# Kernel optimization log

Measured on AMD Instinct MI355X. Metric: run time of the kernel, lower is better.

Reference implementation:

```python
import jax, jax.numpy as jnp
import numpy as np

ALPHA = 0.5
BETA = 0.25
D_AGG = 0.5          # delta_aggregation
D_DIS = 3.0          # delta_discrimination
OHEM_RATIO = 3.0
MAX_INST = 8         # max instance label (labels in 1..MAX_INST, 0 = background)
SMOOTH = 1e-3


def _aggr_discr(text, kernel, embed):
    # text, kernel: [HW] int32 instance labels; embed: [4, HW] float
    inst = jnp.arange(1, MAX_INST + 1)                              # [I]
    kmask = (kernel[None, :] == inst[:, None]).astype(embed.dtype)  # [I, HW]
    tmask = (text[None, :] == inst[:, None]).astype(embed.dtype)   # [I, HW]
    kcnt = kmask.sum(1)                                             # [I]
    tcnt = tmask.sum(1)
    valid = ((kcnt > 0) & (tcnt > 0)).astype(embed.dtype)           # [I]
    # per-instance kernel-mean embedding (segment mean)
    avgs = (kmask @ embed.T) / jnp.maximum(kcnt, 1.0)[:, None]      # [I, 4]
    # aggregation: per-pixel distance to the mean of its text instance
    avgs_full = jnp.concatenate([jnp.zeros((1, 4), embed.dtype), avgs], 0)  # row 0 = bg
    pix_avg = avgs_full[text]                                       # [HW, 4]
    sq = jnp.sum((embed.T - pix_avg) ** 2, axis=1)
    dist = jnp.sqrt(sq + 1e-12) - D_AGG
    lg = jnp.log1p(jnp.maximum(dist, 0.0) ** 2)                     # [HW]
    aggr_i = (tmask @ lg) / jnp.maximum(tcnt, 1.0)                  # [I]
    n = valid.sum()
    loss_aggr = jnp.where(n > 0, (aggr_i * valid).sum() / jnp.maximum(n, 1.0), 0.0)
    # discrimination: pairwise hinge between valid kernel means
    pairv = jnp.triu(valid[:, None] * valid[None, :], k=1)          # [I, I]
    sq_ij = jnp.sum((avgs[:, None, :] - avgs[None, :, :]) ** 2, axis=-1)
    d_ij = jnp.sqrt(jnp.where(pairv > 0, sq_ij, 1.0))               # safe sqrt
    L = jnp.log1p(jnp.maximum(D_DIS - d_ij, 0.0) ** 2)
    denom = n * (n - 1)
    loss_discr = jnp.where(n > 1, (L * pairv).sum() / jnp.maximum(denom, 1.0), 0.0)
    return loss_aggr, loss_discr


def _ohem(score, gt_text, gt_mask):
    # score, gt_text, gt_mask: [HW] float
    pos = gt_text > 0.5
    maskpos = gt_mask > 0.5
    pos_num = (pos & maskpos).sum()
    neg = ~pos
    neg_num = jnp.minimum((pos_num * OHEM_RATIO).astype(jnp.int32), neg.sum())
    neg_sc = jnp.where(neg, score, -jnp.inf)
    srt = -jnp.sort(-neg_sc)                                        # descending
    thr = srt[jnp.clip(neg_num - 1, 0, score.shape[0] - 1)]
    samp = ((score >= thr) | pos) & maskpos
    fallback = (pos_num == 0) | (neg_num == 0)
    return jnp.where(fallback, maskpos, samp).astype(score.dtype)


def _dice(pred_logits, target, mask):
    # all [N, HW]
    p = jax.nn.sigmoid(pred_logits) * mask
    t = (target > 0.5).astype(p.dtype) * mask
    a = jnp.sum(p * t, 1) + SMOOTH
    b = jnp.sum(p * p, 1) + SMOOTH
    c = jnp.sum(t * t, 1) + SMOOTH
    return 1.0 - 2.0 * a / (b + c)


def reference(preds, gt_texts, gt_kernels, gt_mask):
    N, C, H, W = preds.shape
    HW = H * W
    pred_text = preds[:, 0].reshape(N, HW)
    pred_kernel = preds[:, 1].reshape(N, HW)
    embed = preds[:, 2:].reshape(N, 4, HW)
    t = gt_texts.reshape(N, HW)
    k = gt_kernels.reshape(N, HW)
    m = gt_mask.reshape(N, HW).astype(preds.dtype)
    tf = t.astype(preds.dtype)
    kf = k.astype(preds.dtype)
    loss_aggr, loss_discr = jax.vmap(_aggr_discr)(t, k, embed)
    samp = jax.vmap(_ohem)(jax.lax.stop_gradient(pred_text), tf, m)
    loss_text = _dice(pred_text, tf, samp)
    samp_k = (tf > 0.5).astype(preds.dtype) * m
    loss_kernel = _dice(pred_kernel, kf, samp_k)
    # reduction='mean' then coefs [1, alpha, beta, beta]
    return jnp.stack([
        loss_text.mean(),
        ALPHA * loss_kernel.mean(),
        BETA * loss_aggr.mean(),
        BETA * loss_discr.mean(),
    ])


def setup_inputs() -> dict:
    key = jax.random.key(0)
    k1, k2, k3, k4 = jax.random.split(key, 4)
    N, H, W = 16, 512, 512
    preds = jax.random.normal(k1, (N, 6, H, W), dtype=jnp.float32)
    gt_texts = jax.random.randint(k2, (N, H, W), 0, 9, dtype=jnp.int32)
    gt_kernels = jax.random.randint(k3, (N, H, W), 0, 9, dtype=jnp.int32)
    gt_mask = jax.random.randint(k4, (N, H, W), 0, 2, dtype=jnp.int32)
    return {"preds": preds, "gt_texts": gt_texts, "gt_kernels": gt_kernels, "gt_mask": gt_mask}
```

## Files before the change

kernel.cpp:

```cpp
#include <hip/hip_runtime.h>
#include <math.h>

#define HW (512 * 512)
#define NB 16
#define NTHR 256
#define GXS_S 128
#define CH_S 2
#define GXS_P 64
#define CH_P 4
#define ACCW 56

#define OFF_ACC    0
#define OFF_PPART  (OFF_ACC + NB * GXS_S * ACCW)
#define OFF_KDICE  (OFF_PPART + NB * GXS_P * 4)
#define OFF_NVAL   (OFF_KDICE + NB * 3)
#define OFF_DISCR  (OFF_NVAL + NB)


__device__ __forceinline__ unsigned fmap(float f) {
    unsigned u = __float_as_uint(f);
    return (u & 0x80000000u) ? ~u : (u | 0x80000000u);
}
__device__ __forceinline__ float funmap(unsigned u) {
    return (u & 0x80000000u) ? __uint_as_float(u & 0x7FFFFFFFu)
                             : __uint_as_float(~u);
}
__device__ __forceinline__ float wred(float x) {
#pragma unroll
    for (int o = 32; o; o >>= 1) x += __shfl_xor(x, o);
    return x;
}
__device__ __forceinline__ unsigned long long wredull(unsigned long long x) {
#pragma unroll
    for (int o = 32; o; o >>= 1)
        x += (unsigned long long)__shfl_xor((unsigned long long)x, o);
    return x;
}

__global__ __launch_bounds__(NTHR, 2) void k_stats(const float* __restrict__ preds,
                        const int* __restrict__ text,
                        const int* __restrict__ kern,
                        const int* __restrict__ mask,
                        unsigned* __restrict__ wsu) {
    float* wsf = (float*)wsu;
    const int b = blockIdx.y;
    const int tid = threadIdx.x;
    const int lane = tid & 63;
    __shared__ float sacc[53];
    if (tid < 53) sacc[tid] = 0.f;
    __syncthreads();

    const int* tb = text + b * HW;
    const int* kb = kern + b * HW;
    const int* mb = mask + b * HW;
    const float* p1 = preds + (size_t)(b * 6 + 1) * HW;
    const float* e0 = preds + (size_t)(b * 6 + 2) * HW;
    const float* e1 = e0 + HW;
    const float* e2 = e0 + 2 * HW;
    const float* e3 = e0 + 3 * HW;

    unsigned negc = 0u;

    float ks[32];
#pragma unroll
    for (int i = 0; i < 32; i++) ks[i] = 0.f;
    float r_ak = 0.f, r_bk = 0.f, r_ck = 0.f, r_pos = 0.f;
    unsigned kcW[8] = {0, 0, 0, 0, 0, 0, 0, 0};
    unsigned long long tpack = 0ull;

#pragma unroll 1
    for (int c = 0; c < CH_S; c++) {
        const int base = blockIdx.x * (NTHR * 4 * CH_S) + c * (NTHR * 4) + tid * 4;
        const int4 t4 = *(const int4*)(tb + base);
        const int4 k4 = *(const int4*)(kb + base);
        const int4 m4 = *(const int4*)(mb + base);
        const float4 q4 = *(const float4*)(p1 + base);
        const float4 a4 = *(const float4*)(e0 + base);
        const float4 b4 = *(const float4*)(e1 + base);
        const float4 c4 = *(const float4*)(e2 + base);
        const float4 d4 = *(const float4*)(e3 + base);

#define PIX(T, K, M, Q, A, B, C, D) do {                                     \
        bool pos_ = (T) > 0, mp_ = (M) > 0;                                  \
        float sm_ = (pos_ && mp_) ? 1.f : 0.f;                               \
        float sg_ = 1.f / (1.f + expf(-(Q)));                                \
        float ik_ = ((K) > 0) ? 1.f : 0.f;                                   \
        r_ak += sm_ * sg_ * ik_;                                             \
        r_bk += sm_ * sg_ * sg_;                                             \
        r_ck += sm_ * ik_;                                                   \
        r_pos += sm_;                                                        \
        tpack += pos_ ? (1ull << ((((unsigned)(T) - 1u) & 7u) * 8u)) : 0ull; \
        _Pragma("unroll")                                                    \
        for (int i_ = 0; i_ < 8; i_++) {                                     \
            bool hit_ = ((K) == i_ + 1);                                     \
            kcW[i_] += (unsigned)__popcll(__ballot(hit_));                   \
            float h_ = hit_ ? 1.f : 0.f;                                     \
            ks[i_ * 4 + 0] += h_ * (A);                                      \
            ks[i_ * 4 + 1] += h_ * (B);                                      \
            ks[i_ * 4 + 2] += h_ * (C);                                      \
            ks[i_ * 4 + 3] += h_ * (D);                                      \
        }                                                                    \
    } while (0)

        PIX(t4.x, k4.x, m4.x, q4.x, a4.x, b4.x, c4.x, d4.x);
        PIX(t4.y, k4.y, m4.y, q4.y, a4.y, b4.y, c4.y, d4.y);
        PIX(t4.z, k4.z, m4.z, q4.z, a4.z, b4.z, c4.z, d4.z);
        PIX(t4.w, k4.w, m4.w, q4.w, a4.w, b4.w, c4.w, d4.w);
#undef PIX

        negc += (unsigned)(t4.x == 0) + (unsigned)(t4.y == 0)
              + (unsigned)(t4.z == 0) + (unsigned)(t4.w == 0);
    }

#pragma unroll
    for (int i = 0; i < 32; i++) {
        float v = wred(ks[i]);
        if (lane == 0) atomicAdd(&sacc[16 + i], v);
    }
    {
        float v = wred(r_ak); if (lane == 0) atomicAdd(&sacc[49], v);
        v = wred(r_bk); if (lane == 0) atomicAdd(&sacc[50], v);
        v = wred(r_ck); if (lane == 0) atomicAdd(&sacc[51], v);
        v = wred(r_pos); if (lane == 0) atomicAdd(&sacc[48], v);
        unsigned nv = negc;
#pragma unroll
        for (int o = 32; o; o >>= 1) nv += (unsigned)__shfl_xor((int)nv, o);
        if (lane == 0) atomicAdd(&sacc[52], (float)nv);
    }
    {
        unsigned long long lo = tpack & 0x00FF00FF00FF00FFull;
        unsigned long long hi = (tpack >> 8) & 0x00FF00FF00FF00FFull;
        lo = wredull(lo);
        hi = wredull(hi);
        if (lane == 0) {
            atomicAdd(&sacc[8 + 0], (float)(unsigned)( lo        & 0xFFFFull));
            atomicAdd(&sacc[8 + 2], (float)(unsigned)((lo >> 16) & 0xFFFFull));
            atomicAdd(&sacc[8 + 4], (float)(unsigned)((lo >> 32) & 0xFFFFull));
            atomicAdd(&sacc[8 + 6], (float)(unsigned)((lo >> 48) & 0xFFFFull));
            atomicAdd(&sacc[8 + 1], (float)(unsigned)( hi        & 0xFFFFull));
            atomicAdd(&sacc[8 + 3], (float)(unsigned)((hi >> 16) & 0xFFFFull));
            atomicAdd(&sacc[8 + 5], (float)(unsigned)((hi >> 32) & 0xFFFFull));
            atomicAdd(&sacc[8 + 7], (float)(unsigned)((hi >> 48) & 0xFFFFull));
        }
    }
    if (lane == 0) {
#pragma unroll
        for (int i = 0; i < 8; i++) atomicAdd(&sacc[i], (float)kcW[i]);
    }
    __syncthreads();
    if (tid < 53)
        wsf[OFF_ACC + (b * GXS_S + blockIdx.x) * ACCW + tid] = sacc[tid];
}

__global__ __launch_bounds__(NTHR, 2) void k_pix(const float* __restrict__ preds,
                      const int* __restrict__ text,
                      const int* __restrict__ mask,
                      unsigned* __restrict__ wsu) {
    float* wsf = (float*)wsu;
    const int b = blockIdx.y;
    const int tid = threadIdx.x;
    const int lane = tid & 63;
    __shared__ float s_sum[53];
    __shared__ float stbl[45];
    __shared__ int s_valid[8];
    __shared__ float s_thr;
    __shared__ int s_uni;
    __shared__ unsigned s_kk, s_prefix;
    __shared__ unsigned s_hist[256];
    __shared__ float sred[4];

    const int* tb = text + b * HW;
    const int* mb = mask + b * HW;
    const float* p0 = preds + (size_t)(b * 6) * HW;
    const float* e0 = preds + (size_t)(b * 6 + 2) * HW;
    const float* e1 = e0 + HW;
    const float* e2 = e0 + 2 * HW;
    const float* e3 = e0 + 3 * HW;

    if (tid < 53) {
        float v = 0.f;
        const float* p = wsf + OFF_ACC + (size_t)b * GXS_S * ACCW + tid;
        for (int r = 0; r < GXS_S; r++) v += p[r * ACCW];
        s_sum[tid] = v;
    }
    if (tid < 4) sred[tid] = 0.f;
    __syncthreads();
    if (tid < 8) {
        float kcf = s_sum[tid];
        float tcf = s_sum[8 + tid];
        int valid = (kcf > 0.f && tcf > 0.f) ? 1 : 0;
        s_valid[tid] = valid;
        float inv = 1.f / fmaxf(kcf, 1.f);
        float w = valid ? 1.f / fmaxf(tcf, 1.f) : 0.f;
#pragma unroll
        for (int c = 0; c < 4; c++)
            stbl[(tid + 1) * 5 + c] = s_sum[16 + tid * 4 + c] * inv;
        stbl[(tid + 1) * 5 + 4] = w;
    }
    if (tid >= 8 && tid < 13) stbl[tid - 8] = 0.f;
    __syncthreads();
    if (tid == 0) {
        unsigned pos = (unsigned)s_sum[48];
        unsigned neg = (unsigned)s_sum[52];
        unsigned nn = min(pos * 3u, neg);
        int uni = (pos == 0u || nn == 0u || nn == neg) ? 1 : 0;
        s_uni = uni;
        s_kk = uni ? 0u : nn;
        s_thr = 0.f;
        s_prefix = 0u;
    }
    if (blockIdx.x == 0) {
        if (tid >= 16 && tid < 19)
            wsf[OFF_KDICE + b * 3 + (tid - 16)] = s_sum[49 + (tid - 16)];
        if (tid == 32) {
            int nval = 0;
            for (int i = 0; i < 8; i++) nval += s_valid[i];
            wsu[OFF_NVAL + b] = (unsigned)nval;
            float L = 0.f;
            for (int i = 0; i < 8; i++)
                for (int j = i + 1; j < 8; j++)
                    if (s_valid[i] && s_valid[j]) {
                        float sq = 0.f;
                        for (int c = 0; c < 4; c++) {
                            float d = stbl[(i + 1) * 5 + c] - stbl[(j + 1) * 5 + c];
                            sq += d * d;
                        }
                        float h = fmaxf(3.0f - sqrtf(sq), 0.f);
                        L += log1pf(h * h);
                    }
            wsf[OFF_DISCR + b] = (nval > 1) ? L / fmaxf((float)(nval * (nval - 1)), 1.f) : 0.f;
        }
    }
    __syncthreads();
    if (s_kk != 0u) {
        unsigned prefix = 0u;
        for (int pass = 0; pass < 4; pass++) {
            const int shift = 24 - 8 * pass;
            const unsigned fmask = (pass == 0) ? 0u : (0xFFFFFFFFu << (shift + 8));
            s_hist[tid] = 0u;
            __syncthreads();
            for (int p = tid; p < HW; p += NTHR) {
                if (tb[p] == 0) {
                    unsigned key = fmap(p0[p]);
                    if ((key & fmask) == prefix) atomicAdd(&s_hist[(key >> shift) & 255u], 1u);
                }
            }
            __syncthreads();
            if (tid == 0) {
                unsigned k2 = s_kk;
                for (int bin = 255; bin >= 0; --bin) {
                    unsigned c = s_hist[bin];
                    if (k2 <= c) { s_prefix = prefix | (((unsigned)bin) << shift); s_kk = k2; break; }
                    k2 -= c;
                }
            }
            __syncthreads();
            prefix = s_prefix;
        }
        if (tid == 0) s_thr = funmap(prefix);
        __syncthreads();
    }
    const float thr = s_thr;
    const bool uni = s_uni != 0;

    float r_at = 0.f, r_bt = 0.f, r_ct = 0.f, r_ag = 0.f;
#pragma unroll 1
    for (int c = 0; c < CH_P; c++) {
        const int base = blockIdx.x * (NTHR * 4 * CH_P) + c * (NTHR * 4) + tid * 4;
        const int4 t4 = *(const int4*)(tb + base);
        const int4 m4 = *(const int4*)(mb + base);
        const float4 s4 = *(const float4*)(p0 + base);
        const float4 a4 = *(const float4*)(e0 + base);
        const float4 b4 = *(const float4*)(e1 + base);
        const float4 c4 = *(const float4*)(e2 + base);
        const float4 d4 = *(const float4*)(e3 + base);

#define PPIX(T, M, S, A, B, C, D) do {                                       \
        bool pos_ = (T) > 0;                                                 \
        bool samp_ = uni ? ((M) > 0) : ((((S) >= thr) || pos_) && ((M) > 0)); \
        float sg_ = 1.f / (1.f + expf(-(S)));                                \
        float smf_ = samp_ ? 1.f : 0.f;                                      \
        float it_ = pos_ ? 1.f : 0.f;                                        \
        r_at += smf_ * sg_ * it_;                                            \
        r_bt += smf_ * sg_ * sg_;                                            \
        r_ct += smf_ * it_;                                                  \
        int t5_ = min((T), 8) * 5;                                           \
        float d0_ = (A) - stbl[t5_ + 0];                                     \
        float d1_ = (B) - stbl[t5_ + 1];                                     \
        float d2_ = (C) - stbl[t5_ + 2];                                     \
        float d3_ = (D) - stbl[t5_ + 3];                                     \
        float w_ = stbl[t5_ + 4];                                            \
        float sq_ = d0_ * d0_ + d1_ * d1_ + d2_ * d2_ + d3_ * d3_;           \
        float dist_ = sqrtf(sq_ + 1e-12f) - 0.5f;                            \
        float hp_ = fmaxf(dist_, 0.f);                                       \
        r_ag += w_ * log1pf(hp_ * hp_);                                      \
    } while (0)

        PPIX(t4.x, m4.x, s4.x, a4.x, b4.x, c4.x, d4.x);
        PPIX(t4.y, m4.y, s4.y, a4.y, b4.y, c4.y, d4.y);
        PPIX(t4.z, m4.z, s4.z, a4.z, b4.z, c4.z, d4.z);
        PPIX(t4.w, m4.w, s4.w, a4.w, b4.w, c4.w, d4.w);
#undef PPIX
    }

    {
        float v = wred(r_at); if (lane == 0) atomicAdd(&sred[0], v);
        v = wred(r_bt); if (lane == 0) atomicAdd(&sred[1], v);
        v = wred(r_ct); if (lane == 0) atomicAdd(&sred[2], v);
        v = wred(r_ag); if (lane == 0) atomicAdd(&sred[3], v);
    }
    __syncthreads();
    if (tid < 4)
        wsf[OFF_PPART + (b * GXS_P + blockIdx.x) * 4 + tid] = sred[tid];
}

__global__ void k_final(unsigned* __restrict__ wsu, float* __restrict__ out) {
    float* wsf = (float*)wsu;
    __shared__ float sfin[64];
    __shared__ float lt[NB], lk[NB], la[NB], ld[NB];
    const int tid = threadIdx.x;
    {
        const int bb = tid >> 2, v = tid & 3;
        float s = 0.f;
        const float* p = wsf + OFF_PPART + (size_t)bb * GXS_P * 4 + v;
        for (int r = 0; r < GXS_P; r++) s += p[r * 4];
        sfin[tid] = s;
    }
    __syncthreads();
    if (tid < NB) {
        const float S = 1e-3f;
        float at = sfin[tid * 4 + 0], bt = sfin[tid * 4 + 1];
        float ct = sfin[tid * 4 + 2], ag = sfin[tid * 4 + 3];
        float ak = wsf[OFF_KDICE + tid * 3 + 0];
        float bk = wsf[OFF_KDICE + tid * 3 + 1];
        float ck = wsf[OFF_KDICE + tid * 3 + 2];
        lt[tid] = 1.f - 2.f * (at + S) / ((bt + S) + (ct + S));
        lk[tid] = 1.f - 2.f * (ak + S) / ((bk + S) + (ck + S));
        int nval = (int)wsu[OFF_NVAL + tid];
        la[tid] = (nval > 0) ? ag / fmaxf((float)nval, 1.f) : 0.f;
        ld[tid] = wsf[OFF_DISCR + tid];
    }
    __syncthreads();
    if (tid == 0) {
        float st = 0, sk = 0, sa = 0, sd = 0;
        for (int i = 0; i < NB; i++) { st += lt[i]; sk += lk[i]; sa += la[i]; sd += ld[i]; }
        out[0] = st / NB;
        out[1] = 0.5f * sk / NB;
        out[2] = 0.25f * sa / NB;
        out[3] = 0.25f * sd / NB;
    }
}

extern "C" void kernel_launch(void* const* d_in, const int* in_sizes, int n_in,
                              void* d_out, int out_size, void* d_ws, size_t ws_size,
                              hipStream_t stream) {
    const float* preds = (const float*)d_in[0];
    const int* text = (const int*)d_in[1];
    const int* kern = (const int*)d_in[2];
    const int* mask = (const int*)d_in[3];
    unsigned* wsu = (unsigned*)d_ws;
    float* out = (float*)d_out;

    dim3 grid_s(GXS_S, NB);
    dim3 grid_p(GXS_P, NB);
    k_stats<<<grid_s, NTHR, 0, stream>>>(preds, text, kern, mask, wsu);
    k_pix<<<grid_p, NTHR, 0, stream>>>(preds, text, mask, wsu);
    k_final<<<1, 64, 0, stream>>>(wsu, out);
}
```

Before: 228.3 us.

## Move text dice sums into stats pass when OHEM selects all negatives

The text-dice partial sums for the case where OHEM keeps every masked pixel are now computed in the first stats kernel, which reads the text score channel in addition to its other inputs. The second pixel kernel gets a branch for that case that only loads text labels and embeddings for the aggregation term, skipping the mask and score loads and the sigmoid. The final kernel adds the precomputed text-dice sums from a new workspace slot. In exchange, the stats kernel does an extra channel load and a second sigmoid per pixel on every input, including inputs that take the non-uniform path.

Measured after the change: 233.1 us. 2.1% more time.

```diff
diff --git a/kernel.cpp b/kernel.cpp
--- a/kernel.cpp
+++ b/kernel.cpp
@@ -13,7 +13,8 @@
 #define OFF_ACC    0
 #define OFF_PPART  (OFF_ACC + NB * GXS_S * ACCW)
 #define OFF_KDICE  (OFF_PPART + NB * GXS_P * 4)
-#define OFF_NVAL   (OFF_KDICE + NB * 3)
+#define OFF_TDICE  (OFF_KDICE + NB * 3)
+#define OFF_NVAL   (OFF_TDICE + NB * 3)
 #define OFF_DISCR  (OFF_NVAL + NB)
 
 
@@ -46,13 +47,14 @@
     const int b = blockIdx.y;
     const int tid = threadIdx.x;
     const int lane = tid & 63;
-    __shared__ float sacc[53];
-    if (tid < 53) sacc[tid] = 0.f;
+    __shared__ float sacc[55];
+    if (tid < 55) sacc[tid] = 0.f;
     __syncthreads();
 
     const int* tb = text + b * HW;
     const int* kb = kern + b * HW;
     const int* mb = mask + b * HW;
+    const float* p0 = preds + (size_t)(b * 6 + 0) * HW;
     const float* p1 = preds + (size_t)(b * 6 + 1) * HW;
     const float* e0 = preds + (size_t)(b * 6 + 2) * HW;
     const float* e1 = e0 + HW;
@@ -65,6 +67,7 @@
 #pragma unroll
     for (int i = 0; i < 32; i++) ks[i] = 0.f;
     float r_ak = 0.f, r_bk = 0.f, r_ck = 0.f, r_pos = 0.f;
+    float r_at = 0.f, r_bt = 0.f;
     unsigned kcW[8] = {0, 0, 0, 0, 0, 0, 0, 0};
     unsigned long long tpack = 0ull;
 
@@ -74,21 +77,26 @@
         const int4 t4 = *(const int4*)(tb + base);
         const int4 k4 = *(const int4*)(kb + base);
         const int4 m4 = *(const int4*)(mb + base);
+        const float4 s4 = *(const float4*)(p0 + base);
         const float4 q4 = *(const float4*)(p1 + base);
         const float4 a4 = *(const float4*)(e0 + base);
         const float4 b4 = *(const float4*)(e1 + base);
         const float4 c4 = *(const float4*)(e2 + base);
         const float4 d4 = *(const float4*)(e3 + base);
 
-#define PIX(T, K, M, Q, A, B, C, D) do {                                     \
+#define PIX(T, K, M, Q, S, A, B, C, D) do {                                  \
         bool pos_ = (T) > 0, mp_ = (M) > 0;                                  \
         float sm_ = (pos_ && mp_) ? 1.f : 0.f;                               \
+        float mpf_ = mp_ ? 1.f : 0.f;                                        \
         float sg_ = 1.f / (1.f + expf(-(Q)));                                \
+        float sg0_ = 1.f / (1.f + expf(-(S)));                               \
         float ik_ = ((K) > 0) ? 1.f : 0.f;                                   \
         r_ak += sm_ * sg_ * ik_;                                             \
         r_bk += sm_ * sg_ * sg_;                                             \
         r_ck += sm_ * ik_;                                                   \
         r_pos += sm_;                                                        \
+        r_at += sm_ * sg0_;                                                  \
+        r_bt += mpf_ * sg0_ * sg0_;                                          \
         tpack += pos_ ? (1ull << ((((unsigned)(T) - 1u) & 7u) * 8u)) : 0ull; \
         _Pragma("unroll")                                                    \
         for (int i_ = 0; i_ < 8; i_++) {                                     \
@@ -102,10 +110,10 @@
         }                                                                    \
     } while (0)
 
-        PIX(t4.x, k4.x, m4.x, q4.x, a4.x, b4.x, c4.x, d4.x);
-        PIX(t4.y, k4.y, m4.y, q4.y, a4.y, b4.y, c4.y, d4.y);
-        PIX(t4.z, k4.z, m4.z, q4.z, a4.z, b4.z, c4.z, d4.z);
-        PIX(t4.w, k4.w, m4.w, q4.w, a4.w, b4.w, c4.w, d4.w);
+        PIX(t4.x, k4.x, m4.x, q4.x, s4.x, a4.x, b4.x, c4.x, d4.x);
+        PIX(t4.y, k4.y, m4.y, q4.y, s4.y, a4.y, b4.y, c4.y, d4.y);
+        PIX(t4.z, k4.z, m4.z, q4.z, s4.z, a4.z, b4.z, c4.z, d4.z);
+        PIX(t4.w, k4.w, m4.w, q4.w, s4.w, a4.w, b4.w, c4.w, d4.w);
 #undef PIX
 
         negc += (unsigned)(t4.x == 0) + (unsigned)(t4.y == 0)
@@ -122,6 +130,8 @@
         v = wred(r_bk); if (lane == 0) atomicAdd(&sacc[50], v);
         v = wred(r_ck); if (lane == 0) atomicAdd(&sacc[51], v);
         v = wred(r_pos); if (lane == 0) atomicAdd(&sacc[48], v);
+        v = wred(r_at); if (lane == 0) atomicAdd(&sacc[53], v);
+        v = wred(r_bt); if (lane == 0) atomicAdd(&sacc[54], v);
         unsigned nv = negc;
 #pragma unroll
         for (int o = 32; o; o >>= 1) nv += (unsigned)__shfl_xor((int)nv, o);
@@ -148,7 +158,7 @@
         for (int i = 0; i < 8; i++) atomicAdd(&sacc[i], (float)kcW[i]);
     }
     __syncthreads();
-    if (tid < 53)
+    if (tid < 55)
         wsf[OFF_ACC + (b * GXS_S + blockIdx.x) * ACCW + tid] = sacc[tid];
 }
 
@@ -160,7 +170,7 @@
     const int b = blockIdx.y;
     const int tid = threadIdx.x;
     const int lane = tid & 63;
-    __shared__ float s_sum[53];
+    __shared__ float s_sum[55];
     __shared__ float stbl[45];
     __shared__ int s_valid[8];
     __shared__ float s_thr;
@@ -177,7 +187,7 @@
     const float* e2 = e0 + 2 * HW;
     const float* e3 = e0 + 3 * HW;
 
-    if (tid < 53) {
+    if (tid < 55) {
         float v = 0.f;
         const float* p = wsf + OFF_ACC + (size_t)b * GXS_S * ACCW + tid;
         for (int r = 0; r < GXS_S; r++) v += p[r * ACCW];
@@ -209,9 +219,15 @@
         s_thr = 0.f;
         s_prefix = 0u;
     }
+    __syncthreads();
     if (blockIdx.x == 0) {
         if (tid >= 16 && tid < 19)
             wsf[OFF_KDICE + b * 3 + (tid - 16)] = s_sum[49 + (tid - 16)];
+        if (tid >= 20 && tid < 23) {
+            const int idx[3] = {53, 54, 48};
+            wsf[OFF_TDICE + b * 3 + (tid - 20)] =
+                s_uni ? s_sum[idx[tid - 20]] : 0.f;
+        }
         if (tid == 32) {
             int nval = 0;
             for (int i = 0; i < 8; i++) nval += s_valid[i];
@@ -264,20 +280,50 @@
     const bool uni = s_uni != 0;
 
     float r_at = 0.f, r_bt = 0.f, r_ct = 0.f, r_ag = 0.f;
+    if (uni) {
 #pragma unroll 1
-    for (int c = 0; c < CH_P; c++) {
-        const int base = blockIdx.x * (NTHR * 4 * CH_P) + c * (NTHR * 4) + tid * 4;
-        const int4 t4 = *(const int4*)(tb + base);
-        const int4 m4 = *(const int4*)(mb + base);
-        const float4 s4 = *(const float4*)(p0 + base);
-        const float4 a4 = *(const float4*)(e0 + base);
-        const float4 b4 = *(const float4*)(e1 + base);
-        const float4 c4 = *(const float4*)(e2 + base);
-        const float4 d4 = *(const float4*)(e3 + base);
+        for (int c = 0; c < CH_P; c++) {
+            const int base = blockIdx.x * (NTHR * 4 * CH_P) + c * (NTHR * 4) + tid * 4;
+            const int4 t4 = *(const int4*)(tb + base);
+            const float4 a4 = *(const float4*)(e0 + base);
+            const float4 b4 = *(const float4*)(e1 + base);
+            const float4 c4 = *(const float4*)(e2 + base);
+            const float4 d4 = *(const float4*)(e3 + base);
+
+#define AGPIX(T, A, B, C, D) do {                                            \
+        int t5_ = min((T), 8) * 5;                                           \
+        float d0_ = (A) - stbl[t5_ + 0];                                     \
+        float d1_ = (B) - stbl[t5_ + 1];                                     \
+        float d2_ = (C) - stbl[t5_ + 2];                                     \
+        float d3_ = (D) - stbl[t5_ + 3];                                     \
+        float w_ = stbl[t5_ + 4];                                            \
+        float sq_ = d0_ * d0_ + d1_ * d1_ + d2_ * d2_ + d3_ * d3_;           \
+        float dist_ = sqrtf(sq_ + 1e-12f) - 0.5f;                            \
+        float hp_ = fmaxf(dist_, 0.f);                                       \
+        r_ag += w_ * log1pf(hp_ * hp_);                                      \
+    } while (0)
+
+            AGPIX(t4.x, a4.x, b4.x, c4.x, d4.x);
+            AGPIX(t4.y, a4.y, b4.y, c4.y, d4.y);
+            AGPIX(t4.z, a4.z, b4.z, c4.z, d4.z);
+            AGPIX(t4.w, a4.w, b4.w, c4.w, d4.w);
+#undef AGPIX
+        }
+    } else {
+#pragma unroll 1
+        for (int c = 0; c < CH_P; c++) {
+            const int base = blockIdx.x * (NTHR * 4 * CH_P) + c * (NTHR * 4) + tid * 4;
+            const int4 t4 = *(const int4*)(tb + base);
+            const int4 m4 = *(const int4*)(mb + base);
+            const float4 s4 = *(const float4*)(p0 + base);
+            const float4 a4 = *(const float4*)(e0 + base);
+            const float4 b4 = *(const float4*)(e1 + base);
+            const float4 c4 = *(const float4*)(e2 + base);
+            const float4 d4 = *(const float4*)(e3 + base);
 
 #define PPIX(T, M, S, A, B, C, D) do {                                       \
         bool pos_ = (T) > 0;                                                 \
-        bool samp_ = uni ? ((M) > 0) : ((((S) >= thr) || pos_) && ((M) > 0)); \
+        bool samp_ = (((S) >= thr) || pos_) && ((M) > 0);                    \
         float sg_ = 1.f / (1.f + expf(-(S)));                                \
         float smf_ = samp_ ? 1.f : 0.f;                                      \
         float it_ = pos_ ? 1.f : 0.f;                                        \
@@ -296,11 +342,12 @@
         r_ag += w_ * log1pf(hp_ * hp_);                                      \
     } while (0)
 
-        PPIX(t4.x, m4.x, s4.x, a4.x, b4.x, c4.x, d4.x);
-        PPIX(t4.y, m4.y, s4.y, a4.y, b4.y, c4.y, d4.y);
-        PPIX(t4.z, m4.z, s4.z, a4.z, b4.z, c4.z, d4.z);
-        PPIX(t4.w, m4.w, s4.w, a4.w, b4.w, c4.w, d4.w);
+            PPIX(t4.x, m4.x, s4.x, a4.x, b4.x, c4.x, d4.x);
+            PPIX(t4.y, m4.y, s4.y, a4.y, b4.y, c4.y, d4.y);
+            PPIX(t4.z, m4.z, s4.z, a4.z, b4.z, c4.z, d4.z);
+            PPIX(t4.w, m4.w, s4.w, a4.w, b4.w, c4.w, d4.w);
 #undef PPIX
+        }
     }
 
     {
@@ -324,6 +371,7 @@
         float s = 0.f;
         const float* p = wsf + OFF_PPART + (size_t)bb * GXS_P * 4 + v;
         for (int r = 0; r < GXS_P; r++) s += p[r * 4];
+        if (v < 3) s += wsf[OFF_TDICE + bb * 3 + v];
         sfin[tid] = s;
     }
     __syncthreads();
```
